# Optimization experiments

Hardware: AMD Instinct MI355X
Metric: run time of the kernel (lower is better)

## Reference

```python
import jax, jax.numpy as jnp
import numpy as np

B, N, L, F = 8, 256, 48, 96

def setup_inputs() -> dict:
    key = jax.random.key(0)
    k1, k2 = jax.random.split(key)
    x = jax.random.normal(k1, (B, N, N, L), dtype=jnp.float32)
    w = jax.random.normal(k2, (15, L, F), dtype=jnp.float32) * 0.05  # 'random_normal' init
    return {"x": x, "w": w}

def reference(x, w):
    # x: [B, N, N, L], w: [15, L, F]
    Bn, Nn, _, Ln = x.shape
    totsum = jnp.einsum('bijl->bl', x)          # [B, L]
    trace  = jnp.einsum('biil->bl', x)          # [B, L]
    diag   = jnp.einsum('biil->bil', x)         # [B, N, L]
    rowsum = jnp.einsum('bijl->bil', x)         # sum over j -> [B, N, L] (index i)
    colsum = jnp.einsum('bijl->bjl', x)         # sum over i -> [B, N, L] (index j)

    # Diagonal-placed terms (res0..res4): delta_ij * (node part + scalar part)
    diag_node = (jnp.einsum('bil,lf->bif', diag,   w[0])
               + jnp.einsum('bil,lf->bif', rowsum, w[1])
               + jnp.einsum('bil,lf->bif', colsum, w[2]))          # [B, N, F]
    diag_scal = trace @ w[3] + totsum @ w[4]                        # [B, F]
    eye = jnp.eye(Nn, dtype=x.dtype)
    out = (eye[None, :, :, None] * diag_node[:, :, None, :]
         + eye[None, :, :, None] * diag_scal[:, None, None, :])    # [B, N, N, F]

    # Broadcast over i (res5..res7: vector indexed by j)
    bj = (jnp.einsum('bjl,lf->bjf', diag,   w[5])
        + jnp.einsum('bjl,lf->bjf', rowsum, w[6])
        + jnp.einsum('bjl,lf->bjf', colsum, w[7]))                 # [B, N, F]
    out = out + bj[:, None, :, :]

    # Broadcast over j (res8..res10: vector indexed by i)
    bi = (jnp.einsum('bil,lf->bif', diag,   w[8])
        + jnp.einsum('bil,lf->bif', rowsum, w[9])
        + jnp.einsum('bil,lf->bif', colsum, w[10]))                # [B, N, F]
    out = out + bi[:, :, None, :]

    # Dense terms: transpose (res11) and identity (res12)
    out = out + jnp.einsum('bijl,lf->bjif', x, w[11])
    out = out + jnp.einsum('bijl,lf->bijf', x, w[12])

    # Global scalar broadcasts (res13, res14)
    scal = trace @ w[13] + totsum @ w[14]                           # [B, F]
    out = out + scal[:, None, None, :]
    return out
```

## Files before the change

kernel.cpp:

```cpp
#include <hip/hip_runtime.h>

#define Bx 8
#define Nx 256
#define Lx 48
#define Fx 96
#define KK 96
#define KP 104

typedef __attribute__((ext_vector_type(8))) short bf16x8;
typedef __attribute__((ext_vector_type(4))) float f32x4;

__device__ __forceinline__ unsigned short f2bf(float f) {
    unsigned int u = __float_as_uint(f);
    u += 0x7fffu + ((u >> 16) & 1u);
    return (unsigned short)(u >> 16);
}
__device__ __forceinline__ unsigned int pack2(float a, float b) {
    return (unsigned int)f2bf(a) | ((unsigned int)f2bf(b) << 16);
}

__global__ __launch_bounds__(192) void k_row(const float* __restrict__ x,
                                             float* __restrict__ rowsum,
                                             float* __restrict__ diagv) {
    const int blk = blockIdx.x;
    const int t = threadIdx.x;
    const int l = t % Lx;
    const int g = t / Lx;
    __shared__ float red[192];
    const size_t base = (size_t)blk * Nx * Lx;
    float acc = 0.f;
    for (int j = g; j < Nx; j += 4)
        acc += x[base + (size_t)j * Lx + l];
    red[t] = acc;
    __syncthreads();
    if (g == 0)
        rowsum[(size_t)blk * Lx + l] = red[l] + red[48 + l] + red[96 + l] + red[144 + l];
    if (t < Lx)
        diagv[(size_t)blk * Lx + t] = x[base + (size_t)(blk & 255) * Lx + t];
}

__global__ __launch_bounds__(256) void k_col(const float* __restrict__ x,
                                             float* __restrict__ colsum) {
    const int blk = blockIdx.x;
    const int is = blk & 7;
    const int jc = (blk >> 3) & 15;
    const int b  = blk >> 7;
    const int t = threadIdx.x;
    const size_t cb = (size_t)b * Nx * Nx * Lx + (size_t)jc * 16 * Lx;
    float a0 = 0.f, a1 = 0.f, a2 = 0.f;
    for (int ii = 0; ii < 32; ++ii) {
        const int i = is * 32 + ii;
        const float* p = x + cb + (size_t)i * Nx * Lx;
        a0 += p[t];
        a1 += p[t + 256];
        a2 += p[t + 512];
    }
    float* c = colsum + ((size_t)b * Nx + jc * 16) * Lx;
    atomicAdd(c + t, a0);
    atomicAdd(c + t + 256, a1);
    atomicAdd(c + t + 512, a2);
}

__global__ __launch_bounds__(64) void k1b_trace(const float* __restrict__ rowsum,
                                                const float* __restrict__ diagv,
                                                float* __restrict__ trace,
                                                float* __restrict__ totsum) {
    const int b = blockIdx.x;
    const int l = threadIdx.x;
    if (l >= Lx) return;
    float tr = 0.f, ts = 0.f;
    for (int i = 0; i < Nx; ++i) {
        const size_t idx = (size_t)(b * Nx + i) * Lx + l;
        tr += diagv[idx];
        ts += rowsum[idx];
    }
    trace[b * Lx + l]  = tr;
    totsum[b * Lx + l] = ts;
}

__global__ __launch_bounds__(128) void k2_vectors(const float* __restrict__ w,
                                                  const float* __restrict__ rowsum,
                                                  const float* __restrict__ colsum,
                                                  const float* __restrict__ diagv,
                                                  const float* __restrict__ trace,
                                                  const float* __restrict__ totsum,
                                                  float* __restrict__ add_i,
                                                  float* __restrict__ add_j,
                                                  float* __restrict__ add_d) {
    const int blk = blockIdx.x;
    const int b = blk >> 8;
    const int f = threadIdx.x;
    if (f >= Fx) return;

    const float* dP  = diagv  + (size_t)blk * Lx;
    const float* rP  = rowsum + (size_t)blk * Lx;
    const float* cP  = colsum + (size_t)blk * Lx;
    const float* trP = trace  + b * Lx;
    const float* tsP = totsum + b * Lx;

    float ai = 0.f, aj = 0.f, ad = 0.f;
    #pragma unroll 4
    for (int l = 0; l < Lx; ++l) {
        const float d  = dP[l];
        const float r  = rP[l];
        const float c  = cP[l];
        const float tr = trP[l];
        const float ts = tsP[l];
        const float* wl = w + (size_t)l * Fx + f;
        ad = fmaf(d,  wl[0  * Lx * Fx], ad);
        ad = fmaf(r,  wl[1  * Lx * Fx], ad);
        ad = fmaf(c,  wl[2  * Lx * Fx], ad);
        ad = fmaf(tr, wl[3  * Lx * Fx], ad);
        ad = fmaf(ts, wl[4  * Lx * Fx], ad);
        aj = fmaf(d,  wl[5  * Lx * Fx], aj);
        aj = fmaf(r,  wl[6  * Lx * Fx], aj);
        aj = fmaf(c,  wl[7  * Lx * Fx], aj);
        ai = fmaf(d,  wl[8  * Lx * Fx], ai);
        ai = fmaf(r,  wl[9  * Lx * Fx], ai);
        ai = fmaf(c,  wl[10 * Lx * Fx], ai);
        ai = fmaf(tr, wl[13 * Lx * Fx], ai);
        ai = fmaf(ts, wl[14 * Lx * Fx], ai);
    }
    add_i[(size_t)blk * Fx + f] = ai;
    add_j[(size_t)blk * Fx + f] = aj;
    add_d[(size_t)blk * Fx + f] = ad;
}

__global__ __launch_bounds__(256) void k_w(const float* __restrict__ w,
                                           unsigned short* __restrict__ wt) {
    const int idx = blockIdx.x * 256 + threadIdx.x;
    if (idx >= Fx * KP) return;
    const int f = idx / KP, kk = idx % KP;
    float v = 0.f;
    if (kk < 48)      v = w[12 * Lx * Fx + kk * Fx + f];
    else if (kk < 96) v = w[11 * Lx * Fx + (kk - 48) * Fx + f];
    wt[idx] = f2bf(v);
}

__global__ __launch_bounds__(256) void k3_mfma(const float* __restrict__ x,
                                               const unsigned short* __restrict__ wt,
                                               const float* __restrict__ add_i,
                                               const float* __restrict__ add_j,
                                               const float* __restrict__ add_d,
                                               float* __restrict__ out) {
    __shared__ unsigned short Al[64 * KP];
    __shared__ unsigned short Bl[96 * KP];
    const int blk = blockIdx.x;
    const int jt = blk & 3;
    const int bi = blk >> 2;
    const int b  = bi >> 8;
    const int i  = bi & 255;
    const int j0 = jt * 64;
    const int t  = threadIdx.x;

    {
        const uint4* src = (const uint4*)wt;
        uint4* dst = (uint4*)Bl;
        #pragma unroll
        for (int it = 0; it < 5; ++it) {
            const int idx = t + it * 256;
            if (idx < (96 * KP * 2) / 16) dst[idx] = src[idx];
        }
    }
    {
        const int r = t >> 2, q = t & 3;
        const float* pij = x + ((size_t)bi * Nx + j0 + r) * Lx;
        const float* pji = x + ((size_t)(b * Nx + j0 + r) * Nx + i) * Lx;
        unsigned int* arow = (unsigned int*)Al + r * (KP / 2);
        #pragma unroll
        for (int e = 0; e < 3; ++e) {
            const float4 v = *(const float4*)(pij + q * 4 + e * 16);
            arow[q * 2 + e * 8 + 0] = pack2(v.x, v.y);
            arow[q * 2 + e * 8 + 1] = pack2(v.z, v.w);
        }
        #pragma unroll
        for (int e = 0; e < 3; ++e) {
            const float4 v = *(const float4*)(pji + q * 4 + e * 16);
            arow[24 + q * 2 + e * 8 + 0] = pack2(v.x, v.y);
            arow[24 + q * 2 + e * 8 + 1] = pack2(v.z, v.w);
        }
    }
    __syncthreads();

    const int wave = t >> 6, lane = t & 63;
    const int lm = lane & 15, quad = lane >> 4;
    const int m0 = wave * 16;

    bf16x8 afr[3];
    #pragma unroll
    for (int ks = 0; ks < 3; ++ks)
        afr[ks] = *(const bf16x8*)(Al + (m0 + lm) * KP + ks * 32 + quad * 8);

    f32x4 acc[6];
    #pragma unroll
    for (int nt = 0; nt < 6; ++nt) {
        f32x4 c = {0.f, 0.f, 0.f, 0.f};
        #pragma unroll
        for (int ks = 0; ks < 3; ++ks) {
            const bf16x8 bfr = *(const bf16x8*)(Bl + (nt * 16 + lm) * KP + ks * 32 + quad * 8);
            c = __builtin_amdgcn_mfma_f32_16x16x32_bf16(afr[ks], bfr, c, 0, 0, 0);
        }
        acc[nt] = c;
    }

    const float* aiP = add_i + (size_t)bi * Fx;
    const float* adP = add_d + (size_t)bi * Fx;
    float* outP = out + (size_t)bi * Nx * Fx;
    #pragma unroll
    for (int nt = 0; nt < 6; ++nt) {
        const int f = nt * 16 + lm;
        const float ai = aiP[f];
        #pragma unroll
        for (int reg = 0; reg < 4; ++reg) {
            const int j = j0 + m0 + quad * 4 + reg;
            float v = acc[nt][reg] + ai + add_j[((size_t)(b * Nx) + j) * Fx + f];
            if (j == i) v += adP[f];
            outP[(size_t)j * Fx + f] = v;
        }
    }
}

extern "C" void kernel_launch(void* const* d_in, const int* in_sizes, int n_in,
                              void* d_out, int out_size, void* d_ws, size_t ws_size,
                              hipStream_t stream) {
    const float* x = (const float*)d_in[0];
    const float* w = (const float*)d_in[1];
    float* out = (float*)d_out;

    float* ws      = (float*)d_ws;
    float* rowsum  = ws;
    float* colsum  = rowsum + (size_t)Bx * Nx * Lx;
    float* diagv   = colsum + (size_t)Bx * Nx * Lx;
    float* trace   = diagv  + (size_t)Bx * Nx * Lx;
    float* totsum  = trace  + (size_t)Bx * Lx;
    float* add_i   = totsum + (size_t)Bx * Lx;
    float* add_j   = add_i  + (size_t)Bx * Nx * Fx;
    float* add_d   = add_j  + (size_t)Bx * Nx * Fx;
    unsigned short* wtbf = (unsigned short*)(add_d + (size_t)Bx * Nx * Fx);

    k_row<<<Bx * Nx, 192, 0, stream>>>(x, rowsum, diagv);
    hipMemsetAsync(colsum, 0, (size_t)Bx * Nx * Lx * sizeof(float), stream);
    k_col<<<Bx * 16 * 8, 256, 0, stream>>>(x, colsum);
    k1b_trace<<<Bx, 64, 0, stream>>>(rowsum, diagv, trace, totsum);
    k2_vectors<<<Bx * Nx, 128, 0, stream>>>(w, rowsum, colsum, diagv, trace, totsum,
                                            add_i, add_j, add_d);
    k_w<<<(Fx * KP + 255) / 256, 256, 0, stream>>>(w, wtbf);
    k3_mfma<<<Bx * Nx * 4, 256, 0, stream>>>(x, wtbf, add_i, add_j, add_d, out);
}
```

Baseline: 409.7 us.

## Fuse row/col reductions and process symmetric (i,j)/(j,i) tile pairs together

The separate row-sum and column-sum kernels become one pass over x. That pass accumulates column sums in registers, row sums via LDS atomics and picks up the diagonal on the way. The main MFMA kernel now walks upper-triangular 16x16 (i,j) tile pairs. Each pair loads x[i,j] and x[j,i] once and produces both output tiles by swapping the K halves of the A operand. This aims to cut global reads of x from about three passes to two. The costs are more LDS use per block, fewer blocks, LDS atomic contention, and weights now read from global or cache instead of LDS.

```diff
diff --git a/kernel.cpp b/kernel.cpp
--- a/kernel.cpp
+++ b/kernel.cpp
@@ -4,7 +4,6 @@
 #define Nx 256
 #define Lx 48
 #define Fx 96
-#define KK 96
 #define KP 104
 
 typedef __attribute__((ext_vector_type(8))) short bf16x8;
@@ -19,46 +18,57 @@
     return (unsigned int)f2bf(a) | ((unsigned int)f2bf(b) << 16);
 }
 
-__global__ __launch_bounds__(192) void k_row(const float* __restrict__ x,
-                                             float* __restrict__ rowsum,
-                                             float* __restrict__ diagv) {
+__global__ __launch_bounds__(256) void k_sums(const float* __restrict__ x,
+                                              float* __restrict__ rowsum,
+                                              float* __restrict__ colsum,
+                                              float* __restrict__ diagv) {
     const int blk = blockIdx.x;
-    const int t = threadIdx.x;
-    const int l = t % Lx;
-    const int g = t / Lx;
-    __shared__ float red[192];
-    const size_t base = (size_t)blk * Nx * Lx;
-    float acc = 0.f;
-    for (int j = g; j < Nx; j += 4)
-        acc += x[base + (size_t)j * Lx + l];
-    red[t] = acc;
+    const int jc = blk & 15;
+    const int is = (blk >> 4) & 7;
+    const int b  = blk >> 7;
+    const int t  = threadIdx.x;
+
+    __shared__ float rs[32 * 48];
+    #pragma unroll
+    for (int k = 0; k < 6; ++k) rs[t + k * 256] = 0.f;
     __syncthreads();
-    if (g == 0)
-        rowsum[(size_t)blk * Lx + l] = red[l] + red[48 + l] + red[96 + l] + red[144 + l];
-    if (t < Lx)
-        diagv[(size_t)blk * Lx + t] = x[base + (size_t)(blk & 255) * Lx + t];
-}
-
-__global__ __launch_bounds__(256) void k_col(const float* __restrict__ x,
-                                             float* __restrict__ colsum) {
-    const int blk = blockIdx.x;
-    const int is = blk & 7;
-    const int jc = (blk >> 3) & 15;
-    const int b  = blk >> 7;
-    const int t = threadIdx.x;
-    const size_t cb = (size_t)b * Nx * Nx * Lx + (size_t)jc * 16 * Lx;
-    float a0 = 0.f, a1 = 0.f, a2 = 0.f;
+
+    const int j0 = (t)       / 48, l0 = (t)       % 48;
+    const int j1 = (t + 256) / 48, l1 = (t + 256) % 48;
+    const int j2 = (t + 512) / 48, l2 = (t + 512) % 48;
+
+    const size_t base = (size_t)b * Nx * Nx * Lx + (size_t)(is * 32) * Nx * Lx
+                      + (size_t)(jc * 16) * Lx;
+    float ca0 = 0.f, ca1 = 0.f, ca2 = 0.f;
+
     for (int ii = 0; ii < 32; ++ii) {
-        const int i = is * 32 + ii;
-        const float* p = x + cb + (size_t)i * Nx * Lx;
-        a0 += p[t];
-        a1 += p[t + 256];
-        a2 += p[t + 512];
-    }
-    float* c = colsum + ((size_t)b * Nx + jc * 16) * Lx;
-    atomicAdd(c + t, a0);
-    atomicAdd(c + t + 256, a1);
-    atomicAdd(c + t + 512, a2);
+        const int ig = is * 32 + ii;
+        const float* p = x + base + (size_t)ii * Nx * Lx;
+        const float v0 = p[t];
+        const float v1 = p[t + 256];
+        const float v2 = p[t + 512];
+        ca0 += v0; ca1 += v1; ca2 += v2;
+        atomicAdd(&rs[ii * 48 + l0], v0);
+        atomicAdd(&rs[ii * 48 + l1], v1);
+        atomicAdd(&rs[ii * 48 + l2], v2);
+        const int jb = jc * 16;
+        if (jb + j0 == ig) diagv[(size_t)(b * Nx + ig) * Lx + l0] = v0;
+        if (jb + j1 == ig) diagv[(size_t)(b * Nx + ig) * Lx + l1] = v1;
+        if (jb + j2 == ig) diagv[(size_t)(b * Nx + ig) * Lx + l2] = v2;
+    }
+
+    float* cs = colsum + ((size_t)b * Nx + jc * 16) * Lx;
+    atomicAdd(cs + t,       ca0);
+    atomicAdd(cs + t + 256, ca1);
+    atomicAdd(cs + t + 512, ca2);
+
+    __syncthreads();
+    #pragma unroll
+    for (int k = 0; k < 6; ++k) {
+        const int idx = t + k * 256;
+        const int ii = idx / 48, l = idx % 48;
+        atomicAdd(&rowsum[(size_t)(b * Nx + is * 32 + ii) * Lx + l], rs[idx]);
+    }
 }
 
 __global__ __launch_bounds__(64) void k1b_trace(const float* __restrict__ rowsum,
@@ -143,79 +153,85 @@
                                                const float* __restrict__ add_j,
                                                const float* __restrict__ add_d,
                                                float* __restrict__ out) {
-    __shared__ unsigned short Al[64 * KP];
-    __shared__ unsigned short Bl[96 * KP];
-    const int blk = blockIdx.x;
-    const int jt = blk & 3;
-    const int bi = blk >> 2;
-    const int b  = bi >> 8;
-    const int i  = bi & 255;
-    const int j0 = jt * 64;
-    const int t  = threadIdx.x;
-
-    {
-        const uint4* src = (const uint4*)wt;
-        uint4* dst = (uint4*)Bl;
-        #pragma unroll
-        for (int it = 0; it < 5; ++it) {
-            const int idx = t + it * 256;
-            if (idx < (96 * KP * 2) / 16) dst[idx] = src[idx];
-        }
-    }
-    {
-        const int r = t >> 2, q = t & 3;
-        const float* pij = x + ((size_t)bi * Nx + j0 + r) * Lx;
-        const float* pji = x + ((size_t)(b * Nx + j0 + r) * Nx + i) * Lx;
-        unsigned int* arow = (unsigned int*)Al + r * (KP / 2);
-        #pragma unroll
-        for (int e = 0; e < 3; ++e) {
-            const float4 v = *(const float4*)(pij + q * 4 + e * 16);
-            arow[q * 2 + e * 8 + 0] = pack2(v.x, v.y);
-            arow[q * 2 + e * 8 + 1] = pack2(v.z, v.w);
-        }
-        #pragma unroll
-        for (int e = 0; e < 3; ++e) {
-            const float4 v = *(const float4*)(pji + q * 4 + e * 16);
-            arow[24 + q * 2 + e * 8 + 0] = pack2(v.x, v.y);
-            arow[24 + q * 2 + e * 8 + 1] = pack2(v.z, v.w);
-        }
+    __shared__ unsigned short Abuf[256 * KP];
+
+    int p = blockIdx.x;
+    int ti = 0;
+    while (p >= 16 - ti) { p -= 16 - ti; ++ti; }
+    const int tj = ti + p;
+    const int b  = blockIdx.y;
+    const int I = ti * 16, J = tj * 16;
+    const int t = threadIdx.x;
+
+    const float* xb = x + (size_t)b * Nx * Nx * Lx;
+
+    #pragma unroll
+    for (int it = 0; it < 12; ++it) {
+        const int flat = it * 256 + t;
+        const int il = flat / 192;
+        const int q  = flat % 192;
+        const int jl = q / 12, l4 = q % 12;
+        const float4 v = *(const float4*)(xb + ((size_t)(I + il) * Nx + (J + jl)) * Lx + l4 * 4);
+        unsigned int* dst = (unsigned int*)Abuf + (il * 16 + jl) * (KP / 2) + l4 * 2;
+        dst[0] = pack2(v.x, v.y);
+        dst[1] = pack2(v.z, v.w);
+    }
+    #pragma unroll
+    for (int it = 0; it < 12; ++it) {
+        const int flat = it * 256 + t;
+        const int jl = flat / 192;
+        const int q  = flat % 192;
+        const int il = q / 12, l4 = q % 12;
+        const float4 v = *(const float4*)(xb + ((size_t)(J + jl) * Nx + (I + il)) * Lx + l4 * 4);
+        unsigned int* dst = (unsigned int*)Abuf + (il * 16 + jl) * (KP / 2) + 24 + l4 * 2;
+        dst[0] = pack2(v.x, v.y);
+        dst[1] = pack2(v.z, v.w);
     }
     __syncthreads();
 
     const int wave = t >> 6, lane = t & 63;
     const int lm = lane & 15, quad = lane >> 4;
-    const int m0 = wave * 16;
-
-    bf16x8 afr[3];
-    #pragma unroll
-    for (int ks = 0; ks < 3; ++ks)
-        afr[ks] = *(const bf16x8*)(Al + (m0 + lm) * KP + ks * 32 + quad * 8);
-
-    f32x4 acc[6];
-    #pragma unroll
-    for (int nt = 0; nt < 6; ++nt) {
-        f32x4 c = {0.f, 0.f, 0.f, 0.f};
+
+    #pragma unroll
+    for (int pass = 0; pass < 2; ++pass) {
         #pragma unroll
-        for (int ks = 0; ks < 3; ++ks) {
-            const bf16x8 bfr = *(const bf16x8*)(Bl + (nt * 16 + lm) * KP + ks * 32 + quad * 8);
-            c = __builtin_amdgcn_mfma_f32_16x16x32_bf16(afr[ks], bfr, c, 0, 0, 0);
-        }
-        acc[nt] = c;
-    }
-
-    const float* aiP = add_i + (size_t)bi * Fx;
-    const float* adP = add_d + (size_t)bi * Fx;
-    float* outP = out + (size_t)bi * Nx * Fx;
-    #pragma unroll
-    for (int nt = 0; nt < 6; ++nt) {
-        const int f = nt * 16 + lm;
-        const float ai = aiP[f];
-        #pragma unroll
-        for (int reg = 0; reg < 4; ++reg) {
-            const int j = j0 + m0 + quad * 4 + reg;
-            float v = acc[nt][reg] + ai + add_j[((size_t)(b * Nx) + j) * Fx + f];
-            if (j == i) v += adP[f];
-            outP[(size_t)j * Fx + f] = v;
+        for (int nt = 0; nt < 6; ++nt) {
+            bf16x8 bfr[3];
+            #pragma unroll
+            for (int ks = 0; ks < 3; ++ks)
+                bfr[ks] = *(const bf16x8*)(wt + (nt * 16 + lm) * KP + ks * 32 + quad * 8);
+
+            f32x4 acc[4];
+            #pragma unroll
+            for (int mi = 0; mi < 4; ++mi) {
+                f32x4 c = {0.f, 0.f, 0.f, 0.f};
+                const int row = (wave * 4 + mi) * 16 + lm;
+                #pragma unroll
+                for (int ks = 0; ks < 3; ++ks) {
+                    int off = ks * 32 + quad * 8;
+                    if (pass) off = (off >= 48) ? off - 48 : off + 48;
+                    const bf16x8 afr = *(const bf16x8*)(Abuf + row * KP + off);
+                    c = __builtin_amdgcn_mfma_f32_16x16x32_bf16(afr, bfr[ks], c, 0, 0, 0);
+                }
+                acc[mi] = c;
+            }
+
+            const int f = nt * 16 + lm;
+            #pragma unroll
+            for (int mi = 0; mi < 4; ++mi) {
+                const int mt = wave * 4 + mi;
+                #pragma unroll
+                for (int reg = 0; reg < 4; ++reg) {
+                    const int jl2 = quad * 4 + reg;
+                    const int i = pass ? (J + jl2) : (I + mt);
+                    const int j = pass ? (I + mt)  : (J + jl2);
+                    float v = acc[mi][reg]
+                            + add_i[(size_t)(b * Nx + i) * Fx + f]
+                            + add_j[(size_t)(b * Nx + j) * Fx + f];
+                    if (i == j) v += add_d[(size_t)(b * Nx + i) * Fx + f];
+                    out[((size_t)(b * Nx + i) * Nx + j) * Fx + f] = v;
+                }
+            }
         }
     }
 }
@@ -238,12 +254,12 @@
     float* add_d   = add_j  + (size_t)Bx * Nx * Fx;
     unsigned short* wtbf = (unsigned short*)(add_d + (size_t)Bx * Nx * Fx);
 
-    k_row<<<Bx * Nx, 192, 0, stream>>>(x, rowsum, diagv);
-    hipMemsetAsync(colsum, 0, (size_t)Bx * Nx * Lx * sizeof(float), stream);
-    k_col<<<Bx * 16 * 8, 256, 0, stream>>>(x, colsum);
+    hipMemsetAsync(rowsum, 0, 2 * (size_t)Bx * Nx * Lx * sizeof(float), stream);
+    k_w<<<(Fx * KP + 255) / 256, 256, 0, stream>>>(w, wtbf);
+    k_sums<<<Bx * 8 * 16, 256, 0, stream>>>(x, rowsum, colsum, diagv);
     k1b_trace<<<Bx, 64, 0, stream>>>(rowsum, diagv, trace, totsum);
     k2_vectors<<<Bx * Nx, 128, 0, stream>>>(w, rowsum, colsum, diagv, trace, totsum,
                                             add_i, add_j, add_d);
-    k_w<<<(Fx * KP + 255) / 256, 256, 0, stream>>>(w, wtbf);
-    k3_mfma<<<Bx * Nx * 4, 256, 0, stream>>>(x, wtbf, add_i, add_j, add_d, out);
-}
+    dim3 g3(136, Bx);
+    k3_mfma<<<g3, 256, 0, stream>>>(x, wtbf, add_i, add_j, add_d, out);
+}
```

Measured after the change: 493.1 us. 1.2x slower.

## Exploit transpose symmetry to compute both (i,j) and (j,i) tiles from one load

Applied to the files above, without the earlier changes.

The main MFMA kernel now iterates only over upper-triangular tile pairs (It<=Jt). It reuses the same staged x[i,j] and x[j,i] rows to produce the output at (i,j) in one pass, and at (j,i) in a second pass by swapping the K halves of the A fragment. This roughly halves the global reads of x and the A-tile staging. The cost is a second MFMA pass per block, strided stores for the transposed output, and an uneven tile mapping.

```diff
diff --git a/kernel.cpp b/kernel.cpp
--- a/kernel.cpp
+++ b/kernel.cpp
@@ -4,7 +4,6 @@
 #define Nx 256
 #define Lx 48
 #define Fx 96
-#define KK 96
 #define KP 104
 
 typedef __attribute__((ext_vector_type(8))) short bf16x8;
@@ -145,12 +144,18 @@
                                                float* __restrict__ out) {
     __shared__ unsigned short Al[64 * KP];
     __shared__ unsigned short Bl[96 * KP];
-    const int blk = blockIdx.x;
-    const int jt = blk & 3;
-    const int bi = blk >> 2;
-    const int b  = bi >> 8;
-    const int i  = bi & 255;
-    const int j0 = jt * 64;
+    const int idx = blockIdx.x;
+    const int b   = blockIdx.y;
+    const int p   = idx >> 6;
+    const int io  = idx & 63;
+    int It, Jt;
+    if (p < 4)      { It = 0; Jt = p; }
+    else if (p < 7) { It = 1; Jt = p - 3; }
+    else if (p < 9) { It = 2; Jt = p - 5; }
+    else            { It = 3; Jt = 3; }
+    const int i  = It * 64 + io;
+    const int J  = Jt * 64;
+    const int bi = b * Nx + i;
     const int t  = threadIdx.x;
 
     {
@@ -158,14 +163,14 @@
         uint4* dst = (uint4*)Bl;
         #pragma unroll
         for (int it = 0; it < 5; ++it) {
-            const int idx = t + it * 256;
-            if (idx < (96 * KP * 2) / 16) dst[idx] = src[idx];
+            const int k = t + it * 256;
+            if (k < (96 * KP * 2) / 16) dst[k] = src[k];
         }
     }
     {
         const int r = t >> 2, q = t & 3;
-        const float* pij = x + ((size_t)bi * Nx + j0 + r) * Lx;
-        const float* pji = x + ((size_t)(b * Nx + j0 + r) * Nx + i) * Lx;
+        const float* pij = x + ((size_t)bi * Nx + J + r) * Lx;
+        const float* pji = x + ((size_t)(b * Nx + J + r) * Nx + i) * Lx;
         unsigned int* arow = (unsigned int*)Al + r * (KP / 2);
         #pragma unroll
         for (int e = 0; e < 3; ++e) {
@@ -186,36 +191,47 @@
     const int lm = lane & 15, quad = lane >> 4;
     const int m0 = wave * 16;
 
-    bf16x8 afr[3];
-    #pragma unroll
-    for (int ks = 0; ks < 3; ++ks)
-        afr[ks] = *(const bf16x8*)(Al + (m0 + lm) * KP + ks * 32 + quad * 8);
-
-    f32x4 acc[6];
-    #pragma unroll
-    for (int nt = 0; nt < 6; ++nt) {
-        f32x4 c = {0.f, 0.f, 0.f, 0.f};
-        #pragma unroll
-        for (int ks = 0; ks < 3; ++ks) {
-            const bf16x8 bfr = *(const bf16x8*)(Bl + (nt * 16 + lm) * KP + ks * 32 + quad * 8);
-            c = __builtin_amdgcn_mfma_f32_16x16x32_bf16(afr[ks], bfr, c, 0, 0, 0);
-        }
-        acc[nt] = c;
-    }
-
     const float* aiP = add_i + (size_t)bi * Fx;
+    const float* ajP = add_j + (size_t)bi * Fx;
     const float* adP = add_d + (size_t)bi * Fx;
     float* outP = out + (size_t)bi * Nx * Fx;
-    #pragma unroll
-    for (int nt = 0; nt < 6; ++nt) {
-        const int f = nt * 16 + lm;
-        const float ai = aiP[f];
-        #pragma unroll
-        for (int reg = 0; reg < 4; ++reg) {
-            const int j = j0 + m0 + quad * 4 + reg;
-            float v = acc[nt][reg] + ai + add_j[((size_t)(b * Nx) + j) * Fx + f];
-            if (j == i) v += adP[f];
-            outP[(size_t)j * Fx + f] = v;
+
+    const int npass = (It == Jt) ? 1 : 2;
+    for (int pass = 0; pass < npass; ++pass) {
+        bf16x8 afr[3];
+        #pragma unroll
+        for (int ks = 0; ks < 3; ++ks) {
+            int off = ks * 32 + quad * 8;
+            if (pass) off = (off < 48) ? off + 48 : off - 48;
+            afr[ks] = *(const bf16x8*)(Al + (m0 + lm) * KP + off);
+        }
+        #pragma unroll
+        for (int nt = 0; nt < 6; ++nt) {
+            f32x4 c = {0.f, 0.f, 0.f, 0.f};
+            #pragma unroll
+            for (int ks = 0; ks < 3; ++ks) {
+                const bf16x8 bfr = *(const bf16x8*)(Bl + (nt * 16 + lm) * KP + ks * 32 + quad * 8);
+                c = __builtin_amdgcn_mfma_f32_16x16x32_bf16(afr[ks], bfr, c, 0, 0, 0);
+            }
+            const int f = nt * 16 + lm;
+            if (pass == 0) {
+                const float ai = aiP[f];
+                #pragma unroll
+                for (int reg = 0; reg < 4; ++reg) {
+                    const int j = J + m0 + quad * 4 + reg;
+                    float v = c[reg] + ai + add_j[((size_t)(b * Nx) + j) * Fx + f];
+                    if (j == i) v += adP[f];
+                    outP[(size_t)j * Fx + f] = v;
+                }
+            } else {
+                const float aj = ajP[f];
+                #pragma unroll
+                for (int reg = 0; reg < 4; ++reg) {
+                    const int row = J + m0 + quad * 4 + reg;
+                    float v = c[reg] + aj + add_i[((size_t)(b * Nx) + row) * Fx + f];
+                    out[((size_t)(b * Nx + row) * Nx + i) * Fx + f] = v;
+                }
+            }
         }
     }
 }
@@ -245,5 +261,6 @@
     k2_vectors<<<Bx * Nx, 128, 0, stream>>>(w, rowsum, colsum, diagv, trace, totsum,
                                             add_i, add_j, add_d);
     k_w<<<(Fx * KP + 255) / 256, 256, 0, stream>>>(w, wtbf);
-    k3_mfma<<<Bx * Nx * 4, 256, 0, stream>>>(x, wtbf, add_i, add_j, add_d, out);
-}
+    dim3 g3(640, Bx);
+    k3_mfma<<<g3, 256, 0, stream>>>(x, wtbf, add_i, add_j, add_d, out);
+}
```

Result: faster. 390.3 us (-4.7%).
